# Kernel tuning notes

Measured on AMD Instinct MI355X. Metric: run time of the kernel, lower is better.

The kernel has to match this reference:

```python
import jax, jax.numpy as jnp
import numpy as np

N_CLASSES = 18
NMS_PRE = 1000   # test_cfg.nms_pre, per level
K_NMS = 500      # per-class candidates entering greedy NMS
SCORE_THR = 0.01
IOU_THR = 0.5
LEVEL_NS = [600000, 300000, 150000, 75000]


def _decode(points, pred):
    # fcaf3d axis-aligned decode: pred = (dx-, dx+, dy-, dy+, dz-, dz+) >= 0
    cx = points[:, 0] + (pred[:, 1] - pred[:, 0]) / 2
    cy = points[:, 1] + (pred[:, 3] - pred[:, 2]) / 2
    cz = points[:, 2] + (pred[:, 5] - pred[:, 4]) / 2
    w = pred[:, 0] + pred[:, 1]
    l = pred[:, 2] + pred[:, 3]
    h = pred[:, 4] + pred[:, 5]
    return jnp.stack([cx, cy, cz, w, l, h], axis=-1)  # [N, 6]


def _iou3d(b):
    # axis-aligned 3D IoU, b: [K,6] (cx,cy,cz,w,l,h) -> [K,K]
    mn = b[:, :3] - b[:, 3:] / 2
    mx = b[:, :3] + b[:, 3:] / 2
    lt = jnp.maximum(mn[:, None, :], mn[None, :, :])
    rb = jnp.minimum(mx[:, None, :], mx[None, :, :])
    inter = jnp.clip(rb - lt, 0.0).prod(-1)
    vol = jnp.clip(mx - mn, 0.0).prod(-1)
    return inter / (vol[:, None] + vol[None, :] - inter + 1e-6)


def _level(centerness, bbox_pred, cls_score, points):
    # fused score: cls.sigmoid() * centerness.sigmoid()
    scores = jax.nn.sigmoid(cls_score) * jax.nn.sigmoid(centerness)  # [N,C]
    max_scores = scores.max(axis=1)
    _, ids = jax.lax.top_k(max_scores, NMS_PRE)  # per-level prefilter
    bboxes = _decode(points[ids], bbox_pred[ids])  # [NMS_PRE, 6]
    return bboxes, scores[ids]


def _nms_class(boxes, scores):
    # boxes [M,6], scores [M] for one class -> greedy NMS on top K_NMS
    valid = scores > SCORE_THR
    s = jnp.where(valid, scores, -1.0)
    sv, order = jax.lax.top_k(s, K_NMS)  # sorted desc
    b = boxes[order]
    v = sv > SCORE_THR
    iou = _iou3d(b)  # [K,K]
    idx = jnp.arange(K_NMS)

    def body(i, sup):
        alive = jnp.logical_not(sup[i])
        return sup | (alive & (iou[i] > IOU_THR) & (idx > i))

    sup = jax.lax.fori_loop(0, K_NMS, body, jnp.logical_not(v))
    keep = jnp.logical_not(sup) & v
    return b, sv, keep


def _forward(levels):
    mlvl_bboxes, mlvl_scores = [], []
    for (cn, bp, cs, pt) in levels:
        b, s = _level(cn, bp, cs, pt)
        mlvl_bboxes.append(b)
        mlvl_scores.append(s)
    bboxes = jnp.concatenate(mlvl_bboxes)  # [4*NMS_PRE, 6]
    scores = jnp.concatenate(mlvl_scores)  # [4*NMS_PRE, C]
    # per-class NMS (vmap over class dim)
    b, sv, keep = jax.vmap(_nms_class, in_axes=(None, 1))(bboxes, scores)
    labels = jnp.broadcast_to(jnp.arange(N_CLASSES, dtype=jnp.int32)[:, None], sv.shape)
    return (b.reshape(-1, 6), sv.reshape(-1), labels.reshape(-1), keep.reshape(-1))


def setup_inputs() -> dict:
    key = jax.random.key(0)
    out = {}
    for li, n in enumerate(LEVEL_NS):
        k1, k2, k3, k4, key = jax.random.split(key, 5)
        out[f'centerness{li}'] = jax.random.normal(k1, (n, 1), jnp.float32)
        out[f'bbox_pred{li}'] = jax.random.uniform(k2, (n, 6), jnp.float32)  # non-negative distances
        out[f'cls_score{li}'] = jax.random.normal(k3, (n, N_CLASSES), jnp.float32)
        out[f'points{li}'] = jax.random.normal(k4, (n, 3), jnp.float32) * 2.0
    return out


def reference(centerness0, bbox_pred0, cls_score0, points0,
              centerness1, bbox_pred1, cls_score1, points1,
              centerness2, bbox_pred2, cls_score2, points2,
              centerness3, bbox_pred3, cls_score3, points3):
    levels = [
        (centerness0, bbox_pred0, cls_score0, points0),
        (centerness1, bbox_pred1, cls_score1, points1),
        (centerness2, bbox_pred2, cls_score2, points2),
        (centerness3, bbox_pred3, cls_score3, points3),
    ]
    return _forward(levels)
```

## Files before the change

kernel.cpp:

```cpp
#include <hip/hip_runtime.h>
#include <math.h>

#define N_CLASSES 18
#define NMS_PRE   1000
#define K_NMS     500
#define POOL      4000
#define LIST_CAP  2048
#define NREP      16
#define NSUB      16
#define SUBCAP    (LIST_CAP/NSUB)
#define IOU_THR   0.5f
#define SCORE_THR 0.01f

typedef unsigned long long ull;

struct Ptrs {
  const float* cent[4];
  const float* bbox[4];
  const float* cls[4];
  const float* pts[4];
  int off[4];
  int ntot;
};

__device__ __forceinline__ unsigned int fsort(float f){
  unsigned int b = __float_as_uint(f);
  return (b & 0x80000000u) ? ~b : (b | 0x80000000u);
}
__device__ __forceinline__ float fsort_inv(unsigned int k){
  unsigned int b = (k & 0x80000000u) ? (k & 0x7FFFFFFFu) : ~k;
  return __uint_as_float(b);
}
__device__ __forceinline__ float sigmoidf_(float x){
  return 1.0f / (1.0f + expf(-x));
}
__device__ __forceinline__ int level_of(int f, const Ptrs& P){
  return (f >= P.off[3]) ? 3 : (f >= P.off[2]) ? 2 : (f >= P.off[1]) ? 1 : 0;
}

__device__ __forceinline__ void gload_lds16(const void* g, void* l){
  __builtin_amdgcn_global_load_lds(
      (const __attribute__((address_space(1))) void*)g,
      (__attribute__((address_space(3))) void*)l, 16, 0, 0);
}

__device__ __forceinline__ ull cx_keep(ull mine, ull part, bool keep_hi){
  ull mx = mine > part ? mine : part;
  ull mn = mine > part ? part : mine;
  return keep_hi ? mx : mn;
}
__device__ __forceinline__ void cxpair(ull &a, ull &b, bool a_hi){
  ull mx = a > b ? a : b;
  ull mn = a > b ? b : a;
  a = a_hi ? mx : mn;
  b = a_hi ? mn : mx;
}

__global__ void __launch_bounds__(256) init_kernel(unsigned int* hist_rep, unsigned int* hist2,
                        unsigned int* scnt, ull* lists, unsigned int* state){
  int tid = blockIdx.x*256 + threadIdx.x;
  int stride = gridDim.x*256;
  for (int j = tid; j < NREP*4*2048; j += stride) hist_rep[j] = 0u;
  for (int j = tid; j < 4*2048; j += stride) hist2[j] = 0u;
  for (int j = tid; j < 4*NSUB*16; j += stride) scnt[j] = 0u;
  for (int j = tid; j < 4*LIST_CAP; j += stride) lists[j] = 0ull;
  if (tid < 4){
    state[2*tid]   = 0u;
    state[2*tid+1] = NMS_PRE;
  }
}

__global__ void __launch_bounds__(256) compute_keys(Ptrs P, unsigned int* keys,
                        unsigned int* hist_rep){
  __shared__ __align__(16) float cls_s[256*N_CLASSES];
  __shared__ unsigned int lh[2048];
  int t = threadIdx.x;
  int f0 = blockIdx.x << 8;
  int f = f0 + t;
  int rep = blockIdx.x & (NREP - 1);
  bool valid = f < P.ntot;
  int fl = min(f0 + 255, P.ntot - 1);
  bool uni = (level_of(f0, P) == level_of(fl, P)) && (f0 + 255 < P.ntot);
  int Lb = level_of(f0, P);

  if (uni){
    const float4* base4 = (const float4*)(P.cls[Lb] + (size_t)(f0 - P.off[Lb]) * N_CLASSES);
#pragma unroll
    for (int k = 0; k < 4; ++k){
      int j = (k << 8) + t;
      gload_lds16(base4 + j, (char*)cls_s + (size_t)j * 16);
    }
    if (t < 128){
      int j = 1024 + t;
      gload_lds16(base4 + j, (char*)cls_s + (size_t)j * 16);
    }
  }
  for (int j = t; j < 2048; j += 256) lh[j] = 0u;
  float m = 0.f, cent = 0.f;
  if (uni){
    cent = P.cent[Lb][f - P.off[Lb]];
  } else if (valid){
    int L = level_of(f, P); int i = f - P.off[L];
    const float* cl = P.cls[L] + (size_t)i * N_CLASSES;
    m = cl[0];
    for (int c = 1; c < N_CLASSES; ++c) m = fmaxf(m, cl[c]);
    cent = P.cent[L][i];
  }
  __syncthreads();

  if (uni){
    const float2* row = (const float2*)(cls_s + t * N_CLASSES);
    float2 v0 = row[0];
    m = fmaxf(v0.x, v0.y);
#pragma unroll
    for (int q = 1; q < 9; ++q){
      float2 v = row[q];
      m = fmaxf(m, fmaxf(v.x, v.y));
    }
  }
  if (valid){
    float s = sigmoidf_(m) * sigmoidf_(cent);
    unsigned int key = fsort(s);
    keys[f] = key;
    unsigned int bin = key >> 21;
    if (uni) atomicAdd(&lh[bin], 1u);
    else     atomicAdd(&hist_rep[((rep*4) + level_of(f, P))*2048 + bin], 1u);
  }
  __syncthreads();
  if (uni){
    unsigned int* hb = hist_rep + ((rep*4) + Lb)*2048;
    for (int j = t; j < 2048; j += 256){
      unsigned int v = lh[j];
      if (v) atomicAdd(&hb[j], v);
    }
  }
}

__global__ void __launch_bounds__(256) hist_level(Ptrs P, const unsigned int* keys,
                        const unsigned int* state, unsigned int* hist2){
  int f = blockIdx.x * 256 + threadIdx.x;
  if (f < P.ntot){
    int L = level_of(f, P);
    unsigned int key = keys[f];
    unsigned int Pfx = state[2*L];
    if ((key >> 21) == (Pfx >> 21))
      atomicAdd(&hist2[L*2048 + ((key >> 10) & 0x7FFu)], 1u);
  }
}

__global__ void __launch_bounds__(512) scan_sel(const unsigned int* src, int nrep,
                        unsigned int* state, int pass){
  __shared__ unsigned int lhist[2048];
  int L = blockIdx.x, t = threadIdx.x;
  for (int j = t; j < 2048; j += 512){
    unsigned int s = 0u;
    for (int r = 0; r < nrep; ++r) s += src[((r*4) + L)*2048 + j];
    lhist[j] = s;
  }
  __syncthreads();
  if (t < 64){
    int lane = t;
    unsigned int krem = state[2*L + 1];
    unsigned int Pfx  = state[2*L];
    unsigned int carry = 0;
    for (int ch = 0; ch < 32; ++ch){
      unsigned int cnt = lhist[2047 - (ch*64 + lane)];
      unsigned int pfx = cnt;
#pragma unroll
      for (int off = 1; off < 64; off <<= 1){
        unsigned int u = __shfl_up(pfx, off);
        if (lane >= off) pfx += u;
      }
      unsigned int C = carry + pfx;
      ull bal = __ballot(C >= krem);
      if (bal){
        int fl2 = __ffsll(bal) - 1;
        unsigned int Cf = __shfl(C, fl2);
        unsigned int cf = __shfl(cnt, fl2);
        if (lane == 0){
          unsigned int b = (unsigned int)(2047 - (ch*64 + fl2));
          state[2*L]     = (pass == 0) ? (b << 21) : (Pfx | (b << 10));
          state[2*L + 1] = krem - (Cf - cf);
        }
        break;
      }
      carry = __shfl(C, 63);
    }
  }
}

__global__ void __launch_bounds__(256) compact_kernel(Ptrs P, const unsigned int* keys,
                        const unsigned int* state, unsigned int* scnt, ull* lists){
  int f = blockIdx.x * 256 + threadIdx.x;
  if (f >= P.ntot) return;
  int L = level_of(f, P);
  unsigned int key = keys[f];
  unsigned int T = state[2*L];
  if (key >= T){
    unsigned int sub = (unsigned int)blockIdx.x & (NSUB - 1);
    unsigned int pos = atomicAdd(&scnt[(L*NSUB + sub)*16], 1u);
    if (pos < SUBCAP){
      unsigned int i = (unsigned int)(f - P.off[L]);
      lists[(size_t)L*LIST_CAP + sub*SUBCAP + pos] = ((ull)key << 32) | (ull)(~i);
    }
  }
}

__global__ void __launch_bounds__(1024) sort_idx(const ull* lists, unsigned int* sidx){
  __shared__ ull buf[LIST_CAP];
  int L = blockIdx.x;
  int t = threadIdx.x;
  int e1 = t + 1024;
  const ull* src = lists + (size_t)L*LIST_CAP;
  ull v0 = src[t];
  ull v1 = src[e1];
  for (int k = 2; k <= 2048; k <<= 1){
    for (int j = k >> 1; j > 0; j >>= 1){
      bool hi0 = (((t  & j) == 0) == ((t  & k) == 0));
      bool hi1 = (((e1 & j) == 0) == ((e1 & k) == 0));
      if (j >= 1024){
        cxpair(v0, v1, hi0);
      } else if (j >= 64){
        __syncthreads();
        buf[t] = v0; buf[e1] = v1;
        __syncthreads();
        ull p0 = buf[t ^ j];
        ull p1 = buf[e1 ^ j];
        v0 = cx_keep(v0, p0, hi0);
        v1 = cx_keep(v1, p1, hi1);
      } else {
        ull p0 = __shfl_xor(v0, j);
        ull p1 = __shfl_xor(v1, j);
        v0 = cx_keep(v0, p0, hi0);
        v1 = cx_keep(v1, p1, hi1);
      }
    }
  }
  if (t < NMS_PRE) sidx[L*NMS_PRE + t] = ~((unsigned int)(v0 & 0xFFFFFFFFu));
}

__global__ void __launch_bounds__(64) gather_decode(Ptrs P, const unsigned int* sidx,
                        float* boxes_pool, float* scores_pool){
  int r = blockIdx.x*64 + threadIdx.x;
  if (r >= POOL) return;
  int L = r / NMS_PRE;
  unsigned int i = sidx[r];
  const float* bp = P.bbox[L] + (size_t)i * 6;
  const float* pp = P.pts[L]  + (size_t)i * 3;
  float p0 = bp[0], p1 = bp[1], p2 = bp[2], p3 = bp[3], p4 = bp[4], p5 = bp[5];
  float cx = pp[0] + (p1 - p0) * 0.5f;
  float cy = pp[1] + (p3 - p2) * 0.5f;
  float cz = pp[2] + (p5 - p4) * 0.5f;
  float w = p0 + p1, l = p2 + p3, h = p4 + p5;
  float* bo = boxes_pool + (size_t)r * 6;
  bo[0] = cx; bo[1] = cy; bo[2] = cz; bo[3] = w; bo[4] = l; bo[5] = h;
  float cs = sigmoidf_(P.cent[L][i]);
  const float* cl = P.cls[L] + (size_t)i * N_CLASSES;
#pragma unroll
  for (int c = 0; c < N_CLASSES; ++c)
    scores_pool[(size_t)c * POOL + r] = sigmoidf_(cl[c]) * cs;
}

__global__ void __launch_bounds__(1024) class_topk(const float* scores_pool, const float* boxes_pool,
                        float* out, float* aabb){
  __shared__ unsigned int keyS[4096];
  __shared__ ull comp[512];
  __shared__ unsigned int histS[256];
  __shared__ unsigned int wsum[16], wpre[16];
  __shared__ unsigned int sP, sK, sCnt;
  int c = blockIdx.x;
  int t = threadIdx.x;
  int w = t >> 6, lane = t & 63;

  for (int j = t; j < 4096; j += 1024){
    unsigned int k = 0u;
    if (j < POOL){
      float s = scores_pool[(size_t)c*POOL + j];
      float sval = (s > SCORE_THR) ? s : -1.0f;
      k = fsort(sval);
    }
    keyS[j] = k;
  }
  if (t == 0){ sP = 0u; sK = K_NMS; sCnt = 0u; }
  __syncthreads();

  for (int pass = 0; pass < 4; ++pass){
    int shift = 24 - 8*pass;
    if (t < 256) histS[t] = 0u;
    __syncthreads();
    unsigned int Pfx = sP;
    for (int j = t; j < 4096; j += 1024){
      unsigned int k = keyS[j];
      if ((((ull)(k ^ Pfx)) >> (shift + 8)) == 0ull)
        atomicAdd(&histS[(k >> shift) & 0xFFu], 1u);
    }
    __syncthreads();
    if (w == 0){
      unsigned int krem = sK;
      unsigned int carry = 0;
      for (int ch = 0; ch < 4; ++ch){
        unsigned int cnt = histS[255 - (ch*64 + lane)];
        unsigned int pfx = cnt;
#pragma unroll
        for (int off = 1; off < 64; off <<= 1){
          unsigned int u = __shfl_up(pfx, off);
          if (lane >= off) pfx += u;
        }
        unsigned int C = carry + pfx;
        ull bal = __ballot(C >= krem);
        if (bal){
          int fl = __ffsll(bal) - 1;
          unsigned int Cf = __shfl(C, fl);
          unsigned int cf = __shfl(cnt, fl);
          if (lane == 0){
            sP = Pfx | ((unsigned int)(255 - (ch*64 + fl)) << shift);
            sK = krem - (Cf - cf);
          }
          break;
        }
        carry = __shfl(C, 63);
      }
    }
    __syncthreads();
  }
  unsigned int T = sP, need = sK;

  unsigned int loc[4]; unsigned int ct = 0;
#pragma unroll
  for (int q = 0; q < 4; ++q){
    unsigned int k = keyS[4*t + q];
    loc[q] = k;
    ct += (k == T) ? 1u : 0u;
  }
  unsigned int inc = ct;
#pragma unroll
  for (int off = 1; off < 64; off <<= 1){
    unsigned int u = __shfl_up(inc, off);
    if (lane >= off) inc += u;
  }
  if (lane == 63) wsum[w] = inc;
  __syncthreads();
  if (t < 16){
    unsigned int v = wsum[t];
    unsigned int pincl = v;
#pragma unroll
    for (int off = 1; off < 16; off <<= 1){
      unsigned int u = __shfl_up(pincl, off);
      if (t >= off) pincl += u;
    }
    wpre[t] = pincl - v;
  }
  __syncthreads();
  unsigned int excl = wpre[w] + (inc - ct);

#pragma unroll
  for (int q = 0; q < 4; ++q){
    unsigned int k = loc[q];
    bool surv = false;
    if (k > T) surv = true;
    else if (k == T){ surv = (excl < need); excl += 1u; }
    if (surv){
      unsigned int pos = atomicAdd(&sCnt, 1u);
      if (pos < 512)
        comp[pos] = ((ull)k << 32) | (ull)(~(unsigned int)(4*t + q));
    }
  }
  __syncthreads();

  ull v0 = 0ull;
  if (t < 512 && t < (int)sCnt) v0 = comp[t];
  for (int k = 2; k <= 512; k <<= 1){
    for (int j = k >> 1; j > 0; j >>= 1){
      if (j >= 64){
        __syncthreads();
        if (t < 512) comp[t] = v0;
        __syncthreads();
        if (t < 512){
          ull p0 = comp[t ^ j];
          bool hi0 = (((t & j) == 0) == ((t & k) == 0));
          v0 = cx_keep(v0, p0, hi0);
        }
      } else {
        if (t < 512){
          ull p0 = __shfl_xor(v0, j);
          bool hi0 = (((t & j) == 0) == ((t & k) == 0));
          v0 = cx_keep(v0, p0, hi0);
        }
      }
    }
  }

  if (t < K_NMS){
    ull cm = v0;
    unsigned int j = ~((unsigned int)(cm & 0xFFFFFFFFu));
    float sval = fsort_inv((unsigned int)(cm >> 32));
    int o = c*K_NMS + t;
    const float* bp = boxes_pool + (size_t)j * 6;
    float b0 = bp[0], b1 = bp[1], b2 = bp[2], b3 = bp[3], b4 = bp[4], b5 = bp[5];
    float* ob = out + (size_t)o * 6;
    ob[0] = b0; ob[1] = b1; ob[2] = b2; ob[3] = b3; ob[4] = b4; ob[5] = b5;
    out[54000 + o] = sval;
    out[63000 + o] = (float)c;
    float mn0 = b0 - b3*0.5f, mx0 = b0 + b3*0.5f;
    float mn1 = b1 - b4*0.5f, mx1 = b1 + b4*0.5f;
    float mn2 = b2 - b5*0.5f, mx2 = b2 + b5*0.5f;
    float vol = fmaxf(mx0 - mn0, 0.f) * fmaxf(mx1 - mn1, 0.f) * fmaxf(mx2 - mn2, 0.f);
    float* ap = aabb + ((size_t)c*512 + t) * 8;
    ap[0] = mn0; ap[1] = mn1; ap[2] = mn2; ap[3] = mx0; ap[4] = mx1; ap[5] = mx2;
    ap[6] = vol; ap[7] = sval;
  }
}

__global__ void __launch_bounds__(512) nms_mask(const float* aabb, ull* maskG, ull* flagsG){
  __shared__ float smn0[512], smn1[512], smn2[512];
  __shared__ float smx0[512], smx1[512], smx2[512];
  __shared__ float svol[512];
  __shared__ ull rowbuf[64*8];
  int c = blockIdx.y, chunk = blockIdx.x;
  int t = threadIdx.x, w = t >> 6, lane = t & 63;
  float mn0 = 0.f, mn1 = 0.f, mn2 = 0.f, mx0 = 0.f, mx1 = 0.f, mx2 = 0.f, vol = 0.f;
  if (t < K_NMS){
    const float* ap = aabb + ((size_t)c*512 + t) * 8;
    mn0 = ap[0]; mn1 = ap[1]; mn2 = ap[2];
    mx0 = ap[3]; mx1 = ap[4]; mx2 = ap[5]; vol = ap[6];
  }
  smn0[t] = mn0; smn1[t] = mn1; smn2[t] = mn2;
  smx0[t] = mx0; smx1[t] = mx1; smx2[t] = mx2;
  svol[t] = vol;
  __syncthreads();
  int i0 = chunk * 64, i1 = min(i0 + 64, K_NMS);
  for (int i = i0; i < i1; ++i){
    float lt0 = fmaxf(smn0[i], mn0), lt1 = fmaxf(smn1[i], mn1), lt2 = fmaxf(smn2[i], mn2);
    float rb0 = fminf(smx0[i], mx0), rb1 = fminf(smx1[i], mx1), rb2 = fminf(smx2[i], mx2);
    float inter = fmaxf(rb0 - lt0, 0.f) * fmaxf(rb1 - lt1, 0.f) * fmaxf(rb2 - lt2, 0.f);
    float denom = svol[i] + vol - inter + 1e-6f;
    bool s = (t < K_NMS) && (t > i) && (inter / denom > IOU_THR);
    ull m = __ballot(s);
    if (lane == 0){
      maskG[((size_t)c*K_NMS + i)*8 + w] = m;
      rowbuf[(i - i0)*8 + w] = m;
    }
  }
  __syncthreads();
  if (t < 64){
    int r = i0 + t;
    bool nz = false;
    if (r < K_NMS){
      ull o = 0ull;
#pragma unroll
      for (int z = 0; z < 8; ++z) o |= rowbuf[t*8 + z];
      nz = (o != 0ull);
    }
    ull bal = __ballot(nz);
    if (t == 0) flagsG[(size_t)c*8 + chunk] = bal;
  }
}

__global__ void __launch_bounds__(512) nms_greedy(const float* aabb, const ull* maskG,
                        const ull* flagsG, float* keep_out){
  __shared__ ull maskS[K_NMS*8];
  __shared__ ull vbitsS[8], remS[8];
  int c = blockIdx.x, t = threadIdx.x, w = t >> 6, lane = t & 63;
  ull flg[8];
#pragma unroll
  for (int q = 0; q < 8; ++q) flg[q] = flagsG[(size_t)c*8 + q];
  for (int j = t; j < K_NMS*8; j += 512) maskS[j] = maskG[(size_t)c*K_NMS*8 + j];
  float sv = (t < K_NMS) ? aabb[((size_t)c*512 + t)*8 + 7] : -1.0f;
  ull vb = __ballot(sv > SCORE_THR);
  if (lane == 0) vbitsS[w] = vb;
  __syncthreads();
  if (w == 0){
    ull rem[8];
#pragma unroll
    for (int q = 0; q < 8; ++q) rem[q] = ~vbitsS[q];
#pragma unroll
    for (int q = 0; q < 8; ++q){
      ull cand = flg[q] & ~rem[q];
      while (cand){
        int b = __ffsll(cand) - 1;
        int i = q*64 + b;
#pragma unroll
        for (int z = 0; z < 8; ++z) rem[z] |= maskS[i*8 + z];
        ull above = (b < 63) ? (~0ull << (b + 1)) : 0ull;
        cand = flg[q] & ~rem[q] & above;
      }
    }
    if (lane == 0){
#pragma unroll
      for (int q = 0; q < 8; ++q) remS[q] = rem[q];
    }
  }
  __syncthreads();
  if (t < K_NMS)
    keep_out[c*K_NMS + t] = ((remS[t >> 6] >> (t & 63)) & 1ull) ? 0.0f : 1.0f;
}

extern "C" void kernel_launch(void* const* d_in, const int* in_sizes, int n_in,
                              void* d_out, int out_size, void* d_ws, size_t ws_size,
                              hipStream_t stream){
  Ptrs P;
  int off = 0;
  for (int L = 0; L < 4; ++L){
    P.cent[L] = (const float*)d_in[4*L + 0];
    P.bbox[L] = (const float*)d_in[4*L + 1];
    P.cls[L]  = (const float*)d_in[4*L + 2];
    P.pts[L]  = (const float*)d_in[4*L + 3];
    P.off[L]  = off;
    off += in_sizes[4*L + 0];
  }
  P.ntot = off;

  char* w = (char*)d_ws;
  size_t o = 0;
  auto alloc = [&](size_t bytes) -> char* {
    char* p = w + o;
    o = (o + bytes + 255) & ~(size_t)255;
    return p;
  };
  unsigned int* keys        = (unsigned int*)alloc((size_t)P.ntot * 4);
  unsigned int* hist_rep    = (unsigned int*)alloc((size_t)NREP * 4 * 2048 * 4);
  unsigned int* hist2       = (unsigned int*)alloc(4 * 2048 * 4);
  unsigned int* state       = (unsigned int*)alloc(4 * 2 * 4);
  unsigned int* scnt        = (unsigned int*)alloc(4 * NSUB * 16 * 4);
  ull* lists                = (ull*)alloc((size_t)4 * LIST_CAP * 8);
  unsigned int* sidx        = (unsigned int*)alloc((size_t)POOL * 4);
  float* boxes_pool         = (float*)alloc((size_t)POOL * 6 * 4);
  float* scores_pool        = (float*)alloc((size_t)N_CLASSES * POOL * 4);
  float* aabb               = (float*)alloc((size_t)N_CLASSES * 512 * 8 * 4);
  ull* maskG                = (ull*)alloc((size_t)N_CLASSES * K_NMS * 8 * 8);
  ull* flagsG               = (ull*)alloc((size_t)N_CLASSES * 8 * 8);

  float* out = (float*)d_out;
  int grid = (P.ntot + 255) / 256;

  init_kernel<<<64, 256, 0, stream>>>(hist_rep, hist2, scnt, lists, state);
  compute_keys<<<grid, 256, 0, stream>>>(P, keys, hist_rep);
  scan_sel<<<4, 512, 0, stream>>>(hist_rep, NREP, state, 0);
  hist_level<<<grid, 256, 0, stream>>>(P, keys, state, hist2);
  scan_sel<<<4, 512, 0, stream>>>(hist2, 1, state, 1);
  compact_kernel<<<grid, 256, 0, stream>>>(P, keys, state, scnt, lists);
  sort_idx<<<4, 1024, 0, stream>>>(lists, sidx);
  gather_decode<<<(POOL + 63)/64, 64, 0, stream>>>(P, sidx, boxes_pool, scores_pool);
  class_topk<<<N_CLASSES, 1024, 0, stream>>>(scores_pool, boxes_pool, out, aabb);
  nms_mask<<<dim3(8, N_CLASSES), 512, 0, stream>>>(aabb, maskG, flagsG);
  nms_greedy<<<N_CLASSES, 512, 0, stream>>>(aabb, maskG, flagsG, out + 72000);
}
```

Before: 266.2 us.

## Fuse front-end selection into one cooperative kernel and drop gather_decode

```diff
diff --git a/kernel.cpp b/kernel.cpp
--- a/kernel.cpp
+++ b/kernel.cpp
@@ -1,5 +1,8 @@
 #include <hip/hip_runtime.h>
+#include <hip/hip_cooperative_groups.h>
 #include <math.h>
+
+namespace cg = cooperative_groups;
 
 #define N_CLASSES 18
 #define NMS_PRE   1000
@@ -54,6 +57,161 @@
   ull mn = a > b ? b : a;
   a = a_hi ? mx : mn;
   b = a_hi ? mn : mx;
+}
+
+__device__ __forceinline__ void scan_body(const unsigned int* src, int nrep,
+        unsigned int* state, int pass, int L, unsigned int* lhist){
+  int t = threadIdx.x;
+  for (int j = t; j < 2048; j += 256){
+    unsigned int s = 0u;
+    if (nrep == NREP){
+#pragma unroll
+      for (int r = 0; r < NREP; ++r) s += src[((r*4) + L)*2048 + j];
+    } else {
+      s = src[L*2048 + j];
+    }
+    lhist[j] = s;
+  }
+  __syncthreads();
+  if (t < 64){
+    int lane = t;
+    unsigned int krem = state[2*L + 1];
+    unsigned int Pfx  = state[2*L];
+    unsigned int carry = 0;
+    for (int ch = 0; ch < 32; ++ch){
+      unsigned int cnt = lhist[2047 - (ch*64 + lane)];
+      unsigned int pfx = cnt;
+#pragma unroll
+      for (int off = 1; off < 64; off <<= 1){
+        unsigned int u = __shfl_up(pfx, off);
+        if (lane >= off) pfx += u;
+      }
+      unsigned int C = carry + pfx;
+      ull bal = __ballot(C >= krem);
+      if (bal){
+        int fl2 = __ffsll(bal) - 1;
+        unsigned int Cf = __shfl(C, fl2);
+        unsigned int cf = __shfl(cnt, fl2);
+        if (lane == 0){
+          unsigned int b = (unsigned int)(2047 - (ch*64 + fl2));
+          state[2*L]     = (pass == 0) ? (b << 21) : (Pfx | (b << 10));
+          state[2*L + 1] = krem - (Cf - cf);
+        }
+        break;
+      }
+      carry = __shfl(C, 63);
+    }
+  }
+  __syncthreads();
+}
+
+__global__ void __launch_bounds__(256, 5) front_kernel(Ptrs P, unsigned int* keys,
+    unsigned int* hist_rep, unsigned int* hist2, unsigned int* state,
+    unsigned int* scnt, ull* lists, int ntiles)
+{
+  cg::grid_group grid = cg::this_grid();
+  __shared__ __align__(16) float cls_s[256*N_CLASSES];
+  __shared__ unsigned int lh[2048];
+  int t = threadIdx.x;
+  int gtid = blockIdx.x*256 + t;
+  int gstr = gridDim.x*256;
+
+  for (int j = gtid; j < NREP*4*2048; j += gstr) hist_rep[j] = 0u;
+  for (int j = gtid; j < 4*2048; j += gstr) hist2[j] = 0u;
+  for (int j = gtid; j < 4*NSUB*16; j += gstr) scnt[j] = 0u;
+  for (int j = gtid; j < 4*LIST_CAP; j += gstr) lists[j] = 0ull;
+  if (gtid < 4){ state[2*gtid] = 0u; state[2*gtid+1] = NMS_PRE; }
+  grid.sync();
+
+  for (int tile = blockIdx.x; tile < ntiles; tile += gridDim.x){
+    int f0 = tile << 8;
+    int f = f0 + t;
+    int rep = tile & (NREP - 1);
+    bool valid = f < P.ntot;
+    int fl = min(f0 + 255, P.ntot - 1);
+    bool uni = (level_of(f0, P) == level_of(fl, P)) && (f0 + 255 < P.ntot);
+    int Lb = level_of(f0, P);
+    if (uni){
+      const float4* base4 = (const float4*)(P.cls[Lb] + (size_t)(f0 - P.off[Lb]) * N_CLASSES);
+#pragma unroll
+      for (int k = 0; k < 4; ++k){
+        int j = (k << 8) + t;
+        gload_lds16(base4 + j, (char*)cls_s + (size_t)j * 16);
+      }
+      if (t < 128){
+        int j = 1024 + t;
+        gload_lds16(base4 + j, (char*)cls_s + (size_t)j * 16);
+      }
+    }
+    for (int j = t; j < 2048; j += 256) lh[j] = 0u;
+    float m = 0.f, cent = 0.f;
+    if (uni){
+      cent = P.cent[Lb][f - P.off[Lb]];
+    } else if (valid){
+      int L = level_of(f, P); int i = f - P.off[L];
+      const float* cl = P.cls[L] + (size_t)i * N_CLASSES;
+      m = cl[0];
+      for (int c = 1; c < N_CLASSES; ++c) m = fmaxf(m, cl[c]);
+      cent = P.cent[L][i];
+    }
+    __syncthreads();
+    if (uni){
+      const float2* row = (const float2*)(cls_s + t * N_CLASSES);
+      float2 v0 = row[0];
+      m = fmaxf(v0.x, v0.y);
+#pragma unroll
+      for (int q = 1; q < 9; ++q){
+        float2 v = row[q];
+        m = fmaxf(m, fmaxf(v.x, v.y));
+      }
+    }
+    if (valid){
+      float s = sigmoidf_(m) * sigmoidf_(cent);
+      unsigned int key = fsort(s);
+      keys[f] = key;
+      unsigned int bin = key >> 21;
+      if (uni) atomicAdd(&lh[bin], 1u);
+      else     atomicAdd(&hist_rep[((rep*4) + level_of(f, P))*2048 + bin], 1u);
+    }
+    __syncthreads();
+    if (uni){
+      unsigned int* hb = hist_rep + ((rep*4) + Lb)*2048;
+      for (int j = t; j < 2048; j += 256){
+        unsigned int v = lh[j];
+        if (v) atomicAdd(&hb[j], v);
+      }
+    }
+    __syncthreads();
+  }
+  grid.sync();
+
+  if (blockIdx.x < 4) scan_body(hist_rep, NREP, state, 0, blockIdx.x, lh);
+  grid.sync();
+
+  for (int f = gtid; f < P.ntot; f += gstr){
+    int L = level_of(f, P);
+    unsigned int key = keys[f];
+    unsigned int Pfx = state[2*L];
+    if ((key >> 21) == (Pfx >> 21))
+      atomicAdd(&hist2[L*2048 + ((key >> 10) & 0x7FFu)], 1u);
+  }
+  grid.sync();
+
+  if (blockIdx.x < 4) scan_body(hist2, 1, state, 1, blockIdx.x, lh);
+  grid.sync();
+
+  for (int f = gtid; f < P.ntot; f += gstr){
+    int L = level_of(f, P);
+    unsigned int key = keys[f];
+    unsigned int T = state[2*L];
+    if (key >= T){
+      unsigned int sub = ((unsigned int)f >> 8) & (NSUB - 1);
+      unsigned int pos = atomicAdd(&scnt[(L*NSUB + sub)*16], 1u);
+      if (pos < SUBCAP)
+        lists[(size_t)L*LIST_CAP + sub*SUBCAP + pos] =
+            ((ull)key << 32) | (ull)(~(unsigned int)(f - P.off[L]));
+    }
+  }
 }
 
 __global__ void __launch_bounds__(256) init_kernel(unsigned int* hist_rep, unsigned int* hist2,
@@ -82,7 +240,6 @@
   int fl = min(f0 + 255, P.ntot - 1);
   bool uni = (level_of(f0, P) == level_of(fl, P)) && (f0 + 255 < P.ntot);
   int Lb = level_of(f0, P);
-
   if (uni){
     const float4* base4 = (const float4*)(P.cls[Lb] + (size_t)(f0 - P.off[Lb]) * N_CLASSES);
 #pragma unroll
@@ -107,7 +264,6 @@
     cent = P.cent[L][i];
   }
   __syncthreads();
-
   if (uni){
     const float2* row = (const float2*)(cls_s + t * N_CLASSES);
     float2 v0 = row[0];
@@ -148,45 +304,10 @@
   }
 }
 
-__global__ void __launch_bounds__(512) scan_sel(const unsigned int* src, int nrep,
+__global__ void __launch_bounds__(256) scan_sel(const unsigned int* src, int nrep,
                         unsigned int* state, int pass){
   __shared__ unsigned int lhist[2048];
-  int L = blockIdx.x, t = threadIdx.x;
-  for (int j = t; j < 2048; j += 512){
-    unsigned int s = 0u;
-    for (int r = 0; r < nrep; ++r) s += src[((r*4) + L)*2048 + j];
-    lhist[j] = s;
-  }
-  __syncthreads();
-  if (t < 64){
-    int lane = t;
-    unsigned int krem = state[2*L + 1];
-    unsigned int Pfx  = state[2*L];
-    unsigned int carry = 0;
-    for (int ch = 0; ch < 32; ++ch){
-      unsigned int cnt = lhist[2047 - (ch*64 + lane)];
-      unsigned int pfx = cnt;
-#pragma unroll
-      for (int off = 1; off < 64; off <<= 1){
-        unsigned int u = __shfl_up(pfx, off);
-        if (lane >= off) pfx += u;
-      }
-      unsigned int C = carry + pfx;
-      ull bal = __ballot(C >= krem);
-      if (bal){
-        int fl2 = __ffsll(bal) - 1;
-        unsigned int Cf = __shfl(C, fl2);
-        unsigned int cf = __shfl(cnt, fl2);
-        if (lane == 0){
-          unsigned int b = (unsigned int)(2047 - (ch*64 + fl2));
-          state[2*L]     = (pass == 0) ? (b << 21) : (Pfx | (b << 10));
-          state[2*L + 1] = krem - (Cf - cf);
-        }
-        break;
-      }
-      carry = __shfl(C, 63);
-    }
-  }
+  scan_body(src, nrep, state, pass, blockIdx.x, lhist);
 }
 
 __global__ void __launch_bounds__(256) compact_kernel(Ptrs P, const unsigned int* keys,
@@ -239,29 +360,7 @@
   if (t < NMS_PRE) sidx[L*NMS_PRE + t] = ~((unsigned int)(v0 & 0xFFFFFFFFu));
 }
 
-__global__ void __launch_bounds__(64) gather_decode(Ptrs P, const unsigned int* sidx,
-                        float* boxes_pool, float* scores_pool){
-  int r = blockIdx.x*64 + threadIdx.x;
-  if (r >= POOL) return;
-  int L = r / NMS_PRE;
-  unsigned int i = sidx[r];
-  const float* bp = P.bbox[L] + (size_t)i * 6;
-  const float* pp = P.pts[L]  + (size_t)i * 3;
-  float p0 = bp[0], p1 = bp[1], p2 = bp[2], p3 = bp[3], p4 = bp[4], p5 = bp[5];
-  float cx = pp[0] + (p1 - p0) * 0.5f;
-  float cy = pp[1] + (p3 - p2) * 0.5f;
-  float cz = pp[2] + (p5 - p4) * 0.5f;
-  float w = p0 + p1, l = p2 + p3, h = p4 + p5;
-  float* bo = boxes_pool + (size_t)r * 6;
-  bo[0] = cx; bo[1] = cy; bo[2] = cz; bo[3] = w; bo[4] = l; bo[5] = h;
-  float cs = sigmoidf_(P.cent[L][i]);
-  const float* cl = P.cls[L] + (size_t)i * N_CLASSES;
-#pragma unroll
-  for (int c = 0; c < N_CLASSES; ++c)
-    scores_pool[(size_t)c * POOL + r] = sigmoidf_(cl[c]) * cs;
-}
-
-__global__ void __launch_bounds__(1024) class_topk(const float* scores_pool, const float* boxes_pool,
+__global__ void __launch_bounds__(1024) class_topk(Ptrs P, const unsigned int* sidx,
                         float* out, float* aabb){
   __shared__ unsigned int keyS[4096];
   __shared__ ull comp[512];
@@ -275,7 +374,9 @@
   for (int j = t; j < 4096; j += 1024){
     unsigned int k = 0u;
     if (j < POOL){
-      float s = scores_pool[(size_t)c*POOL + j];
+      int L = j / NMS_PRE;
+      unsigned int i = sidx[j];
+      float s = sigmoidf_(P.cls[L][(size_t)i * N_CLASSES + c]) * sigmoidf_(P.cent[L][i]);
       float sval = (s > SCORE_THR) ? s : -1.0f;
       k = fsort(sval);
     }
@@ -392,11 +493,18 @@
 
   if (t < K_NMS){
     ull cm = v0;
-    unsigned int j = ~((unsigned int)(cm & 0xFFFFFFFFu));
+    unsigned int jj = ~((unsigned int)(cm & 0xFFFFFFFFu));
     float sval = fsort_inv((unsigned int)(cm >> 32));
     int o = c*K_NMS + t;
-    const float* bp = boxes_pool + (size_t)j * 6;
-    float b0 = bp[0], b1 = bp[1], b2 = bp[2], b3 = bp[3], b4 = bp[4], b5 = bp[5];
+    int L = (int)jj / NMS_PRE;
+    unsigned int i = sidx[jj];
+    const float* bp = P.bbox[L] + (size_t)i * 6;
+    const float* pp = P.pts[L]  + (size_t)i * 3;
+    float p0 = bp[0], p1 = bp[1], p2 = bp[2], p3 = bp[3], p4 = bp[4], p5 = bp[5];
+    float b0 = pp[0] + (p1 - p0) * 0.5f;
+    float b1 = pp[1] + (p3 - p2) * 0.5f;
+    float b2 = pp[2] + (p5 - p4) * 0.5f;
+    float b3 = p0 + p1, b4 = p2 + p3, b5 = p4 + p5;
     float* ob = out + (size_t)o * 6;
     ob[0] = b0; ob[1] = b1; ob[2] = b2; ob[3] = b3; ob[4] = b4; ob[5] = b5;
     out[54000 + o] = sval;
@@ -524,24 +632,48 @@
   unsigned int* scnt        = (unsigned int*)alloc(4 * NSUB * 16 * 4);
   ull* lists                = (ull*)alloc((size_t)4 * LIST_CAP * 8);
   unsigned int* sidx        = (unsigned int*)alloc((size_t)POOL * 4);
-  float* boxes_pool         = (float*)alloc((size_t)POOL * 6 * 4);
-  float* scores_pool        = (float*)alloc((size_t)N_CLASSES * POOL * 4);
   float* aabb               = (float*)alloc((size_t)N_CLASSES * 512 * 8 * 4);
   ull* maskG                = (ull*)alloc((size_t)N_CLASSES * K_NMS * 8 * 8);
   ull* flagsG               = (ull*)alloc((size_t)N_CLASSES * 8 * 8);
 
   float* out = (float*)d_out;
   int grid = (P.ntot + 255) / 256;
-
-  init_kernel<<<64, 256, 0, stream>>>(hist_rep, hist2, scnt, lists, state);
-  compute_keys<<<grid, 256, 0, stream>>>(P, keys, hist_rep);
-  scan_sel<<<4, 512, 0, stream>>>(hist_rep, NREP, state, 0);
-  hist_level<<<grid, 256, 0, stream>>>(P, keys, state, hist2);
-  scan_sel<<<4, 512, 0, stream>>>(hist2, 1, state, 1);
-  compact_kernel<<<grid, 256, 0, stream>>>(P, keys, state, scnt, lists);
+  int ntiles = grid;
+
+  static int coopG = 0;
+  static int use_coop = -1;
+  if (use_coop < 0){
+    int bpc = 0;
+    hipError_t qe = hipOccupancyMaxActiveBlocksPerMultiprocessor(&bpc, front_kernel, 256, 0);
+    if (qe == hipSuccess && bpc > 0){
+      if (bpc > 5) bpc = 5;
+      coopG = bpc * 256;
+      use_coop = 1;
+    } else {
+      use_coop = 0;
+    }
+  }
+
+  bool coop_done = false;
+  if (use_coop == 1){
+    void* args[] = { (void*)&P, (void*)&keys, (void*)&hist_rep, (void*)&hist2,
+                     (void*)&state, (void*)&scnt, (void*)&lists, (void*)&ntiles };
+    hipError_t le = hipLaunchCooperativeKernel(reinterpret_cast<void*>(front_kernel),
+                        dim3(coopG), dim3(256), args, 0, stream);
+    if (le == hipSuccess) coop_done = true;
+    else use_coop = 0;
+  }
+  if (!coop_done){
+    init_kernel<<<64, 256, 0, stream>>>(hist_rep, hist2, scnt, lists, state);
+    compute_keys<<<grid, 256, 0, stream>>>(P, keys, hist_rep);
+    scan_sel<<<4, 256, 0, stream>>>(hist_rep, NREP, state, 0);
+    hist_level<<<grid, 256, 0, stream>>>(P, keys, state, hist2);
+    scan_sel<<<4, 256, 0, stream>>>(hist2, 1, state, 1);
+    compact_kernel<<<grid, 256, 0, stream>>>(P, keys, state, scnt, lists);
+  }
+
   sort_idx<<<4, 1024, 0, stream>>>(lists, sidx);
-  gather_decode<<<(POOL + 63)/64, 64, 0, stream>>>(P, sidx, boxes_pool, scores_pool);
-  class_topk<<<N_CLASSES, 1024, 0, stream>>>(scores_pool, boxes_pool, out, aabb);
+  class_topk<<<N_CLASSES, 1024, 0, stream>>>(P, sidx, out, aabb);
   nms_mask<<<dim3(8, N_CLASSES), 512, 0, stream>>>(aabb, maskG, flagsG);
   nms_greedy<<<N_CLASSES, 512, 0, stream>>>(aabb, maskG, flagsG, out + 72000);
 }
```

Result: slower. 933.5 us (+250.7%).

## Fuse gather/decode, class top-k, NMS mask and greedy NMS into one kernel

Applied to the files above, without the earlier changes.

```diff
diff --git a/kernel.cpp b/kernel.cpp
--- a/kernel.cpp
+++ b/kernel.cpp
@@ -82,7 +82,6 @@
   int fl = min(f0 + 255, P.ntot - 1);
   bool uni = (level_of(f0, P) == level_of(fl, P)) && (f0 + 255 < P.ntot);
   int Lb = level_of(f0, P);
-
   if (uni){
     const float4* base4 = (const float4*)(P.cls[Lb] + (size_t)(f0 - P.off[Lb]) * N_CLASSES);
 #pragma unroll
@@ -107,7 +106,6 @@
     cent = P.cent[L][i];
   }
   __syncthreads();
-
   if (uni){
     const float2* row = (const float2*)(cls_s + t * N_CLASSES);
     float2 v0 = row[0];
@@ -148,13 +146,18 @@
   }
 }
 
-__global__ void __launch_bounds__(512) scan_sel(const unsigned int* src, int nrep,
+__global__ void __launch_bounds__(256) scan_sel(const unsigned int* src, int nrep,
                         unsigned int* state, int pass){
   __shared__ unsigned int lhist[2048];
   int L = blockIdx.x, t = threadIdx.x;
-  for (int j = t; j < 2048; j += 512){
+  for (int j = t; j < 2048; j += 256){
     unsigned int s = 0u;
-    for (int r = 0; r < nrep; ++r) s += src[((r*4) + L)*2048 + j];
+    if (nrep == NREP){
+#pragma unroll
+      for (int r = 0; r < NREP; ++r) s += src[((r*4) + L)*2048 + j];
+    } else {
+      s = src[L*2048 + j];
+    }
     lhist[j] = s;
   }
   __syncthreads();
@@ -239,35 +242,16 @@
   if (t < NMS_PRE) sidx[L*NMS_PRE + t] = ~((unsigned int)(v0 & 0xFFFFFFFFu));
 }
 
-__global__ void __launch_bounds__(64) gather_decode(Ptrs P, const unsigned int* sidx,
-                        float* boxes_pool, float* scores_pool){
-  int r = blockIdx.x*64 + threadIdx.x;
-  if (r >= POOL) return;
-  int L = r / NMS_PRE;
-  unsigned int i = sidx[r];
-  const float* bp = P.bbox[L] + (size_t)i * 6;
-  const float* pp = P.pts[L]  + (size_t)i * 3;
-  float p0 = bp[0], p1 = bp[1], p2 = bp[2], p3 = bp[3], p4 = bp[4], p5 = bp[5];
-  float cx = pp[0] + (p1 - p0) * 0.5f;
-  float cy = pp[1] + (p3 - p2) * 0.5f;
-  float cz = pp[2] + (p5 - p4) * 0.5f;
-  float w = p0 + p1, l = p2 + p3, h = p4 + p5;
-  float* bo = boxes_pool + (size_t)r * 6;
-  bo[0] = cx; bo[1] = cy; bo[2] = cz; bo[3] = w; bo[4] = l; bo[5] = h;
-  float cs = sigmoidf_(P.cent[L][i]);
-  const float* cl = P.cls[L] + (size_t)i * N_CLASSES;
-#pragma unroll
-  for (int c = 0; c < N_CLASSES; ++c)
-    scores_pool[(size_t)c * POOL + r] = sigmoidf_(cl[c]) * cs;
-}
-
-__global__ void __launch_bounds__(1024) class_topk(const float* scores_pool, const float* boxes_pool,
-                        float* out, float* aabb){
-  __shared__ unsigned int keyS[4096];
+__global__ void __launch_bounds__(1024) class_nms(Ptrs P, const unsigned int* sidx,
+                        float* out){
+  __shared__ ull maskS[512*8];
   __shared__ ull comp[512];
+  __shared__ float boxA[8][512];
   __shared__ unsigned int histS[256];
   __shared__ unsigned int wsum[16], wpre[16];
+  __shared__ ull vbitsS[8], flgS[8], remS[8];
   __shared__ unsigned int sP, sK, sCnt;
+  unsigned int* keyS = (unsigned int*)&boxA[0][0];
   int c = blockIdx.x;
   int t = threadIdx.x;
   int w = t >> 6, lane = t & 63;
@@ -275,7 +259,9 @@
   for (int j = t; j < 4096; j += 1024){
     unsigned int k = 0u;
     if (j < POOL){
-      float s = scores_pool[(size_t)c*POOL + j];
+      int L = j / NMS_PRE;
+      unsigned int i = sidx[j];
+      float s = sigmoidf_(P.cls[L][(size_t)i * N_CLASSES + c]) * sigmoidf_(P.cent[L][i]);
       float sval = (s > SCORE_THR) ? s : -1.0f;
       k = fsort(sval);
     }
@@ -389,100 +375,92 @@
       }
     }
   }
-
-  if (t < K_NMS){
-    ull cm = v0;
-    unsigned int j = ~((unsigned int)(cm & 0xFFFFFFFFu));
-    float sval = fsort_inv((unsigned int)(cm >> 32));
-    int o = c*K_NMS + t;
-    const float* bp = boxes_pool + (size_t)j * 6;
-    float b0 = bp[0], b1 = bp[1], b2 = bp[2], b3 = bp[3], b4 = bp[4], b5 = bp[5];
-    float* ob = out + (size_t)o * 6;
-    ob[0] = b0; ob[1] = b1; ob[2] = b2; ob[3] = b3; ob[4] = b4; ob[5] = b5;
-    out[54000 + o] = sval;
-    out[63000 + o] = (float)c;
-    float mn0 = b0 - b3*0.5f, mx0 = b0 + b3*0.5f;
-    float mn1 = b1 - b4*0.5f, mx1 = b1 + b4*0.5f;
-    float mn2 = b2 - b5*0.5f, mx2 = b2 + b5*0.5f;
-    float vol = fmaxf(mx0 - mn0, 0.f) * fmaxf(mx1 - mn1, 0.f) * fmaxf(mx2 - mn2, 0.f);
-    float* ap = aabb + ((size_t)c*512 + t) * 8;
-    ap[0] = mn0; ap[1] = mn1; ap[2] = mn2; ap[3] = mx0; ap[4] = mx1; ap[5] = mx2;
-    ap[6] = vol; ap[7] = sval;
-  }
-}
-
-__global__ void __launch_bounds__(512) nms_mask(const float* aabb, ull* maskG, ull* flagsG){
-  __shared__ float smn0[512], smn1[512], smn2[512];
-  __shared__ float smx0[512], smx1[512], smx2[512];
-  __shared__ float svol[512];
-  __shared__ ull rowbuf[64*8];
-  int c = blockIdx.y, chunk = blockIdx.x;
-  int t = threadIdx.x, w = t >> 6, lane = t & 63;
-  float mn0 = 0.f, mn1 = 0.f, mn2 = 0.f, mx0 = 0.f, mx1 = 0.f, mx2 = 0.f, vol = 0.f;
-  if (t < K_NMS){
-    const float* ap = aabb + ((size_t)c*512 + t) * 8;
-    mn0 = ap[0]; mn1 = ap[1]; mn2 = ap[2];
-    mx0 = ap[3]; mx1 = ap[4]; mx2 = ap[5]; vol = ap[6];
-  }
-  smn0[t] = mn0; smn1[t] = mn1; smn2[t] = mn2;
-  smx0[t] = mx0; smx1[t] = mx1; smx2[t] = mx2;
-  svol[t] = vol;
-  __syncthreads();
-  int i0 = chunk * 64, i1 = min(i0 + 64, K_NMS);
-  for (int i = i0; i < i1; ++i){
-    float lt0 = fmaxf(smn0[i], mn0), lt1 = fmaxf(smn1[i], mn1), lt2 = fmaxf(smn2[i], mn2);
-    float rb0 = fminf(smx0[i], mx0), rb1 = fminf(smx1[i], mx1), rb2 = fminf(smx2[i], mx2);
-    float inter = fmaxf(rb0 - lt0, 0.f) * fmaxf(rb1 - lt1, 0.f) * fmaxf(rb2 - lt2, 0.f);
-    float denom = svol[i] + vol - inter + 1e-6f;
-    bool s = (t < K_NMS) && (t > i) && (inter / denom > IOU_THR);
-    ull m = __ballot(s);
-    if (lane == 0){
-      maskG[((size_t)c*K_NMS + i)*8 + w] = m;
-      rowbuf[(i - i0)*8 + w] = m;
-    }
-  }
-  __syncthreads();
-  if (t < 64){
-    int r = i0 + t;
+  __syncthreads();
+
+  if (t < 512){
+    float mn0 = 0.f, mn1 = 0.f, mn2 = 0.f, mx0 = 0.f, mx1 = 0.f, mx2 = 0.f;
+    float vol = 0.f, sval = -1.0f;
+    if (t < K_NMS){
+      unsigned int jj = ~((unsigned int)(v0 & 0xFFFFFFFFu));
+      sval = fsort_inv((unsigned int)(v0 >> 32));
+      int o = c*K_NMS + t;
+      int L = (int)jj / NMS_PRE;
+      unsigned int i = sidx[jj];
+      const float* bp = P.bbox[L] + (size_t)i * 6;
+      const float* pp = P.pts[L]  + (size_t)i * 3;
+      float p0 = bp[0], p1 = bp[1], p2 = bp[2], p3 = bp[3], p4 = bp[4], p5 = bp[5];
+      float b0 = pp[0] + (p1 - p0) * 0.5f;
+      float b1 = pp[1] + (p3 - p2) * 0.5f;
+      float b2 = pp[2] + (p5 - p4) * 0.5f;
+      float b3 = p0 + p1, b4 = p2 + p3, b5 = p4 + p5;
+      float* ob = out + (size_t)o * 6;
+      ob[0] = b0; ob[1] = b1; ob[2] = b2; ob[3] = b3; ob[4] = b4; ob[5] = b5;
+      out[54000 + o] = sval;
+      out[63000 + o] = (float)c;
+      mn0 = b0 - b3*0.5f; mx0 = b0 + b3*0.5f;
+      mn1 = b1 - b4*0.5f; mx1 = b1 + b4*0.5f;
+      mn2 = b2 - b5*0.5f; mx2 = b2 + b5*0.5f;
+      vol = fmaxf(mx0 - mn0, 0.f) * fmaxf(mx1 - mn1, 0.f) * fmaxf(mx2 - mn2, 0.f);
+    }
+    boxA[0][t] = mn0; boxA[1][t] = mn1; boxA[2][t] = mn2;
+    boxA[3][t] = mx0; boxA[4][t] = mx1; boxA[5][t] = mx2;
+    boxA[6][t] = vol; boxA[7][t] = sval;
+  }
+  __syncthreads();
+
+  {
+    int col = t & 511;
+    float cmn0 = boxA[0][col], cmn1 = boxA[1][col], cmn2 = boxA[2][col];
+    float cmx0 = boxA[3][col], cmx1 = boxA[4][col], cmx2 = boxA[5][col];
+    float cvol = boxA[6][col];
+    bool colv = (col < K_NMS);
+    int half = t >> 9;
+    int w7 = w & 7;
+    for (int i = 0; i < K_NMS; i += 2){
+      int r = i + half;
+      float rmn0 = boxA[0][r], rmn1 = boxA[1][r], rmn2 = boxA[2][r];
+      float rmx0 = boxA[3][r], rmx1 = boxA[4][r], rmx2 = boxA[5][r];
+      float rvol = boxA[6][r];
+      float lt0 = fmaxf(rmn0, cmn0), lt1 = fmaxf(rmn1, cmn1), lt2 = fmaxf(rmn2, cmn2);
+      float rb0 = fminf(rmx0, cmx0), rb1 = fminf(rmx1, cmx1), rb2 = fminf(rmx2, cmx2);
+      float inter = fmaxf(rb0 - lt0, 0.f) * fmaxf(rb1 - lt1, 0.f) * fmaxf(rb2 - lt2, 0.f);
+      float denom = rvol + cvol - inter + 1e-6f;
+      bool s = colv && (col > r) && (inter / denom > IOU_THR);
+      ull m = __ballot(s);
+      if (lane == 0) maskS[r*8 + w7] = m;
+    }
+  }
+  __syncthreads();
+
+  if (t < 512){
     bool nz = false;
-    if (r < K_NMS){
-      ull o = 0ull;
-#pragma unroll
-      for (int z = 0; z < 8; ++z) o |= rowbuf[t*8 + z];
-      nz = (o != 0ull);
+    if (t < K_NMS){
+      ull o8 = 0ull;
+#pragma unroll
+      for (int z = 0; z < 8; ++z) o8 |= maskS[t*8 + z];
+      nz = (o8 != 0ull);
     }
     ull bal = __ballot(nz);
-    if (t == 0) flagsG[(size_t)c*8 + chunk] = bal;
-  }
-}
-
-__global__ void __launch_bounds__(512) nms_greedy(const float* aabb, const ull* maskG,
-                        const ull* flagsG, float* keep_out){
-  __shared__ ull maskS[K_NMS*8];
-  __shared__ ull vbitsS[8], remS[8];
-  int c = blockIdx.x, t = threadIdx.x, w = t >> 6, lane = t & 63;
-  ull flg[8];
-#pragma unroll
-  for (int q = 0; q < 8; ++q) flg[q] = flagsG[(size_t)c*8 + q];
-  for (int j = t; j < K_NMS*8; j += 512) maskS[j] = maskG[(size_t)c*K_NMS*8 + j];
-  float sv = (t < K_NMS) ? aabb[((size_t)c*512 + t)*8 + 7] : -1.0f;
-  ull vb = __ballot(sv > SCORE_THR);
-  if (lane == 0) vbitsS[w] = vb;
-  __syncthreads();
+    if (lane == 0) flgS[w] = bal;
+    ull vbb = __ballot(boxA[7][t] > SCORE_THR);
+    if (lane == 0) vbitsS[w] = vbb;
+  }
+  __syncthreads();
+
   if (w == 0){
     ull rem[8];
 #pragma unroll
     for (int q = 0; q < 8; ++q) rem[q] = ~vbitsS[q];
 #pragma unroll
     for (int q = 0; q < 8; ++q){
-      ull cand = flg[q] & ~rem[q];
+      ull cand = flgS[q] & ~rem[q];
       while (cand){
         int b = __ffsll(cand) - 1;
         int i = q*64 + b;
 #pragma unroll
         for (int z = 0; z < 8; ++z) rem[z] |= maskS[i*8 + z];
         ull above = (b < 63) ? (~0ull << (b + 1)) : 0ull;
-        cand = flg[q] & ~rem[q] & above;
+        cand = flgS[q] & ~rem[q] & above;
       }
     }
     if (lane == 0){
@@ -492,7 +470,7 @@
   }
   __syncthreads();
   if (t < K_NMS)
-    keep_out[c*K_NMS + t] = ((remS[t >> 6] >> (t & 63)) & 1ull) ? 0.0f : 1.0f;
+    out[72000 + c*K_NMS + t] = ((remS[t >> 6] >> (t & 63)) & 1ull) ? 0.0f : 1.0f;
 }
 
 extern "C" void kernel_launch(void* const* d_in, const int* in_sizes, int n_in,
@@ -524,24 +502,16 @@
   unsigned int* scnt        = (unsigned int*)alloc(4 * NSUB * 16 * 4);
   ull* lists                = (ull*)alloc((size_t)4 * LIST_CAP * 8);
   unsigned int* sidx        = (unsigned int*)alloc((size_t)POOL * 4);
-  float* boxes_pool         = (float*)alloc((size_t)POOL * 6 * 4);
-  float* scores_pool        = (float*)alloc((size_t)N_CLASSES * POOL * 4);
-  float* aabb               = (float*)alloc((size_t)N_CLASSES * 512 * 8 * 4);
-  ull* maskG                = (ull*)alloc((size_t)N_CLASSES * K_NMS * 8 * 8);
-  ull* flagsG               = (ull*)alloc((size_t)N_CLASSES * 8 * 8);
 
   float* out = (float*)d_out;
   int grid = (P.ntot + 255) / 256;
 
   init_kernel<<<64, 256, 0, stream>>>(hist_rep, hist2, scnt, lists, state);
   compute_keys<<<grid, 256, 0, stream>>>(P, keys, hist_rep);
-  scan_sel<<<4, 512, 0, stream>>>(hist_rep, NREP, state, 0);
+  scan_sel<<<4, 256, 0, stream>>>(hist_rep, NREP, state, 0);
   hist_level<<<grid, 256, 0, stream>>>(P, keys, state, hist2);
-  scan_sel<<<4, 512, 0, stream>>>(hist2, 1, state, 1);
+  scan_sel<<<4, 256, 0, stream>>>(hist2, 1, state, 1);
   compact_kernel<<<grid, 256, 0, stream>>>(P, keys, state, scnt, lists);
   sort_idx<<<4, 1024, 0, stream>>>(lists, sidx);
-  gather_decode<<<(POOL + 63)/64, 64, 0, stream>>>(P, sidx, boxes_pool, scores_pool);
-  class_topk<<<N_CLASSES, 1024, 0, stream>>>(scores_pool, boxes_pool, out, aabb);
-  nms_mask<<<dim3(8, N_CLASSES), 512, 0, stream>>>(aabb, maskG, flagsG);
-  nms_greedy<<<N_CLASSES, 512, 0, stream>>>(aabb, maskG, flagsG, out + 72000);
-}
+  class_nms<<<N_CLASSES, 1024, 0, stream>>>(P, sidx, out);
+}
```

After: 307.1 us. 1.15x slower.
